# Optimization experiments

Measured on AMD Instinct MI355X. Metric: run time of the kernel, lower is better.

The kernel has to match this reference:

```python
import jax, jax.numpy as jnp
import numpy as np

B, C, H, W = 2, 1024, 64, 64
R, E, HE, T, K = 16, 4, 512, 3, 2


def setup_inputs() -> dict:
    key = jax.random.key(0)
    ks = jax.random.split(key, 12)
    s = 0.02
    return {
        "x": jax.random.normal(ks[0], (B, C, H, W), jnp.float32),
        "t": jax.random.normal(ks[1], (B, C, H, W), jnp.float32),
        "fc_w": jax.random.normal(ks[2], (C, 2 * C), jnp.float32) * s,
        "ln_g": jnp.ones((C,), jnp.float32),
        "ln_b": jnp.zeros((C,), jnp.float32),
        "f1_w1": jax.random.normal(ks[3], (C // R, C), jnp.float32) * s,
        "f1_b1": jnp.zeros((C // R,), jnp.float32),
        "f1_wa": jax.random.normal(ks[4], (C, C // R), jnp.float32) * s,
        "f1_ba": jnp.zeros((C,), jnp.float32),
        "f1_wb": jax.random.normal(ks[5], (C, C // R), jnp.float32) * s,
        "f1_bb": jnp.zeros((C,), jnp.float32),
        "w_gate": jax.random.normal(ks[6], (T, C, E), jnp.float32) * s,
        "e_w1": jax.random.normal(ks[7], (E, C, HE), jnp.float32) * s,
        "e_b1": jnp.zeros((E, HE), jnp.float32),
        "e_w2": jax.random.normal(ks[8], (E, HE, C), jnp.float32) * s,
        "e_b2": jnp.zeros((E, C), jnp.float32),
        "task_index": 1,
    }


def _cv_squared(v):
    eps = 1e-10
    return jnp.var(v, ddof=1) / (jnp.mean(v) ** 2 + eps)


def reference(x, t, fc_w, ln_g, ln_b, f1_w1, f1_b1, f1_wa, f1_ba, f1_wb, f1_bb,
              w_gate, e_w1, e_b1, e_w2, e_b2, task_index):
    b, c, h, w = x.shape
    n = h * w
    # MultiTaskGeneralFusion: SE-style dual-branch channel gating
    s = jnp.mean(x + t, axis=(2, 3))                        # [B, C]
    hid = jax.nn.relu(s @ f1_w1.T + f1_b1)                  # [B, C/r]
    a = hid @ f1_wa.T + f1_ba                               # [B, C]
    bb = hid @ f1_wb.T + f1_bb                              # [B, C]
    wts = jax.nn.softmax(jnp.stack([a, bb], axis=0), axis=0)  # [2, B, C]
    z = wts[0][:, :, None, None] * x + wts[1][:, :, None, None] * t
    # fused linear -> ReLU -> LayerNorm on concatenated tokens
    x3 = x.reshape(b, c, n).transpose(0, 2, 1)              # [B, N, C]
    t3 = t.reshape(b, c, n).transpose(0, 2, 1)
    y = jnp.concatenate([x3, t3], axis=-1)                  # [B, N, 2C]
    y = jax.nn.relu(jnp.einsum('bnd,cd->bnc', y, fc_w))     # [B, N, C]
    mu = jnp.mean(y, axis=-1, keepdims=True)
    var = jnp.mean((y - mu) ** 2, axis=-1, keepdims=True)
    y = (y - mu) * jax.lax.rsqrt(var + 1e-5) * ln_g + ln_b
    yf = y.reshape(b * n, c)                                # [BN, C]
    # MMoE top-k gating (eval mode: no gating noise)
    logits = yf @ w_gate[task_index]                        # [BN, E]
    top_logits, top_idx = jax.lax.top_k(logits, K)          # [BN, K]
    top_gates = jax.nn.softmax(top_logits, axis=-1)
    gates = jnp.zeros_like(logits).at[jnp.arange(b * n)[:, None], top_idx].set(top_gates)
    # dense expert compute, gated combine
    eh = jax.nn.relu(jnp.einsum('nc,ech->neh', yf, e_w1) + e_b1)   # [BN, E, HE]
    eo = jnp.einsum('neh,eho->neo', eh, e_w2) + e_b2               # [BN, E, C]
    ym = jnp.einsum('ne,neo->no', gates, eo)                        # [BN, C]
    importance = gates.sum(axis=0)
    load = (gates > 0).sum(axis=0).astype(jnp.float32)
    aux_loss = _cv_squared(importance) + _cv_squared(load)
    y4 = ym.reshape(b, n, c).transpose(0, 2, 1).reshape(b, c, h, w) + z
    return (y4, aux_loss)
```

## Files before the change

kernel.cpp:

```cpp
#include <hip/hip_runtime.h>
#include <cstddef>
#include <cstdint>

#define B_   2
#define C_   1024
#define N_   4096
#define M_   8192
#define K2_  2048
#define E_   4
#define HE_  512

typedef float f32x4 __attribute__((ext_vector_type(4)));
typedef short bf16x8 __attribute__((ext_vector_type(8)));
typedef _Float16 f16x8 __attribute__((ext_vector_type(8)));
typedef unsigned short u16x8 __attribute__((ext_vector_type(8)));

#define WAITV(N) asm volatile("s_waitcnt vmcnt(" #N ")" ::: "memory")
#define SBAR     __builtin_amdgcn_sched_barrier(0)

static __device__ __forceinline__ unsigned short f2bf(float f) {
  unsigned int u = __float_as_uint(f);
  u = u + 0x7fffu + ((u >> 16) & 1u);
  return (unsigned short)(u >> 16);
}

static __device__ __forceinline__ void gl_lds16(const void* g, void* l) {
  __builtin_amdgcn_global_load_lds(
      (const __attribute__((address_space(1))) void*)(uintptr_t)g,
      (__attribute__((address_space(3))) void*)(unsigned)(uintptr_t)l,
      16, 0, 0);
}

__global__ __launch_bounds__(256) void k_se_gate(const float* __restrict__ s,
                                                 const float* __restrict__ w1, const float* __restrict__ b1,
                                                 const float* __restrict__ wa, const float* __restrict__ ba,
                                                 const float* __restrict__ wb, const float* __restrict__ bbv,
                                                 float* __restrict__ wts0) {
  __shared__ float hid[2][64];
  const int t = threadIdx.x;
  if (t < 128) {
    const int b = t >> 6, r = t & 63;
    float acc = b1[r];
    const float* sp = s + b * C_;
    const float* wp = w1 + r * C_;
    for (int c = 0; c < C_; ++c) acc = fmaf(sp[c], wp[c], acc);
    hid[b][r] = fmaxf(acc, 0.f);
  }
  __syncthreads();
  for (int o = t; o < B_ * C_; o += 256) {
    const int b = o >> 10, c = o & 1023;
    float a = ba[c], bb = bbv[c];
    #pragma unroll 8
    for (int r = 0; r < 64; ++r) {
      const float h = hid[b][r];
      a  = fmaf(h, wa[c * 64 + r], a);
      bb = fmaf(h, wb[c * 64 + r], bb);
    }
    wts0[o] = 1.f / (1.f + expf(bb - a));
  }
}

__global__ __launch_bounds__(256) void k_prep_act(const float* __restrict__ x,
                                                  const float* __restrict__ t,
                                                  _Float16* __restrict__ ah,
                                                  _Float16* __restrict__ am,
                                                  float* __restrict__ spart) {
  __shared__ float tile[64][65];
  const int c0 = blockIdx.x * 64, n0 = blockIdx.y * 64, b = blockIdx.z;
  const float* xb = x + (size_t)b * (C_ * N_);
  const float* tb = t + (size_t)b * (C_ * N_);
  _Float16* ahb = ah + (size_t)b * (N_ * (size_t)K2_);
  _Float16* amb = am + (size_t)b * (N_ * (size_t)K2_);
  const int tid = threadIdx.x;
  const int prow = tid >> 2, pseg = tid & 3;
  float psum = 0.f;
  #pragma unroll
  for (int srcsel = 0; srcsel < 2; ++srcsel) {
    const float* src = srcsel ? tb : xb;
    const int koff = srcsel ? C_ : 0;
    if (srcsel) __syncthreads();
    #pragma unroll
    for (int p = 0; p < 4; ++p) {
      const int f = tid + p * 256;
      const int cr = f >> 4, nq = f & 15;
      const float4 v = *(const float4*)(src + (size_t)(c0 + cr) * N_ + n0 + nq * 4);
      tile[cr][nq * 4 + 0] = v.x; tile[cr][nq * 4 + 1] = v.y;
      tile[cr][nq * 4 + 2] = v.z; tile[cr][nq * 4 + 3] = v.w;
    }
    __syncthreads();
    {
      float a = 0.f;
      #pragma unroll
      for (int u = 0; u < 16; ++u) a += tile[prow][pseg * 16 + u];
      psum += a;
    }
    #pragma unroll
    for (int p = 0; p < 2; ++p) {
      const int f = tid + p * 256;
      const int mr = f >> 3, kq = f & 7;
      f16x8 hv, mv;
      #pragma unroll
      for (int u = 0; u < 8; ++u) {
        const float v = tile[kq * 8 + u][mr] * 64.f;
        const _Float16 h = (_Float16)v;
        hv[u] = h;
        mv[u] = (_Float16)(v - (float)h);
      }
      const size_t off = (size_t)(n0 + mr) * K2_ + koff + c0 + kq * 8;
      *(f16x8*)(ahb + off) = hv;
      *(f16x8*)(amb + off) = mv;
    }
  }
  psum += __shfl_xor(psum, 1);
  psum += __shfl_xor(psum, 2);
  if (pseg == 0)
    spart[((size_t)(b * C_ + c0 + prow)) * 64 + blockIdx.y] = psum;
}

__global__ __launch_bounds__(256) void k_reduce2(const float* __restrict__ spart,
                                                 float* __restrict__ s) {
  const int idx = blockIdx.x * 256 + threadIdx.x;
  const float* p = spart + (size_t)idx * 64;
  float acc = 0.f;
  #pragma unroll
  for (int j = 0; j < 64; ++j) acc += p[j];
  s[idx] = acc * (1.f / (float)N_);
}

__global__ __launch_bounds__(256) void k_prep_fcw(const float* __restrict__ w,
                                                  _Float16* __restrict__ wh,
                                                  _Float16* __restrict__ wm) {
  const size_t i = ((size_t)blockIdx.x * 256 + threadIdx.x) * 8;
  const float4 v0 = *(const float4*)(w + i);
  const float4 v1 = *(const float4*)(w + i + 4);
  const float vv[8] = {v0.x, v0.y, v0.z, v0.w, v1.x, v1.y, v1.z, v1.w};
  f16x8 hv, mv;
  #pragma unroll
  for (int u = 0; u < 8; ++u) {
    const float sv = vv[u] * 4096.f;
    const _Float16 h = (_Float16)sv;
    hv[u] = h;
    mv[u] = (_Float16)(sv - (float)h);
  }
  *(f16x8*)(wh + i) = hv;
  *(f16x8*)(wm + i) = mv;
}

__global__ __launch_bounds__(256) void k_prep_tr(const float* __restrict__ src, long long zs, int srs,
                                                 unsigned short* __restrict__ dst, long long zo, int drs) {
  __shared__ float tile[64][65];
  const int c0 = blockIdx.x * 64, r0 = blockIdx.y * 64, z = blockIdx.z;
  const float* s = src + (size_t)z * zs;
  unsigned short* d = dst + (size_t)z * zo;
  const int tid = threadIdx.x;
  #pragma unroll
  for (int p = 0; p < 4; ++p) {
    const int f = tid + p * 256;
    const int rr = f >> 4, cq = f & 15;
    const float4 v = *(const float4*)(s + (size_t)(r0 + rr) * srs + c0 + cq * 4);
    tile[rr][cq * 4 + 0] = v.x; tile[rr][cq * 4 + 1] = v.y;
    tile[rr][cq * 4 + 2] = v.z; tile[rr][cq * 4 + 3] = v.w;
  }
  __syncthreads();
  #pragma unroll
  for (int p = 0; p < 2; ++p) {
    const int f = tid + p * 256;
    const int cr = f >> 3, rq = f & 7;
    u16x8 o;
    #pragma unroll
    for (int u = 0; u < 8; ++u) o[u] = f2bf(tile[rq * 8 + u][cr]);
    *(u16x8*)(d + (size_t)(c0 + cr) * drs + r0 + rq * 8) = o;
  }
}

__global__ __launch_bounds__(512, 2) void k_fc_mfma(const _Float16* __restrict__ Ah,
                                                    const _Float16* __restrict__ Am,
                                                    const _Float16* __restrict__ Bh,
                                                    const _Float16* __restrict__ Bm,
                                                    float* __restrict__ y) {
  __shared__ __align__(16) char lds[2][49152];
  const int tid = threadIdx.x, w = tid >> 6, l = tid & 63;
  const int flat = blockIdx.x + blockIdx.y * 8;
  const int swz = (flat & 7) * 32 + (flat >> 3);
  const int n0 = (swz & 7) * 128, m0 = (swz >> 3) * 256;
  const int wr = w >> 1, wc = w & 1, lg = l >> 4, lr = l & 15;
  f32x4 acc[4][4] = {};

  auto LDA = [&](char* bufb, const _Float16* src, int roff, int k0, int q) {
    const int chunk = q * 512 + tid;
    const int kg = chunk >> 8, row = chunk & 255;
    gl_lds16(src + (size_t)(m0 + row) * K2_ + k0 + kg * 8,
             bufb + roff + (q * 512 + w * 64) * 16);
  };
  auto LDB = [&](char* bufb, const _Float16* src, int roff, int k0) {
    const int kg = tid >> 7, row = tid & 127;
    gl_lds16(src + (size_t)(n0 + row) * K2_ + k0 + kg * 8,
             bufb + roff + (w * 64) * 16);
  };

  LDA(&lds[0][0], Ah, 0, 0, 0);
  LDA(&lds[0][0], Ah, 0, 0, 1);
  LDB(&lds[0][0], Bh, 32768, 0);
  LDB(&lds[0][0], Bm, 40960, 0);
  LDA(&lds[0][0], Am, 16384, 0, 0);
  LDA(&lds[0][0], Am, 16384, 0, 1);

  f16x8 a_h[4], b_h[4], b_m[4], a_m[4];
  for (int t = 0; t < 63; ++t) {
    const int cur = t & 1;
    const char* bb = &lds[cur][0];
    char* nb = &lds[cur ^ 1][0];
    const int nk = (t + 1) * 32;
    WAITV(3); SBAR;
    __builtin_amdgcn_s_barrier();
    LDA(nb, Ah, 0, nk, 0);
    LDA(nb, Ah, 0, nk, 1);
    #pragma unroll
    for (int i = 0; i < 4; ++i)
      a_h[i] = *(const f16x8*)(bb + (lg * 256 + wr * 64 + i * 16 + lr) * 16);
    #pragma unroll
    for (int j = 0; j < 4; ++j)
      b_h[j] = *(const f16x8*)(bb + 32768 + (lg * 128 + wc * 64 + j * 16 + lr) * 16);
    __builtin_amdgcn_s_setprio(1);
    #pragma unroll
    for (int i = 0; i < 4; ++i)
      #pragma unroll
      for (int j = 0; j < 4; ++j)
        acc[i][j] = __builtin_amdgcn_mfma_f32_16x16x32_f16(a_h[i], b_h[j], acc[i][j], 0, 0, 0);
    __builtin_amdgcn_s_setprio(0);
    WAITV(4); SBAR;
    __builtin_amdgcn_s_barrier();
    LDB(nb, Bh, 32768, nk);
    LDB(nb, Bm, 40960, nk);
    #pragma unroll
    for (int j = 0; j < 4; ++j)
      b_m[j] = *(const f16x8*)(bb + 40960 + (lg * 128 + wc * 64 + j * 16 + lr) * 16);
    __builtin_amdgcn_s_setprio(1);
    #pragma unroll
    for (int i = 0; i < 4; ++i)
      #pragma unroll
      for (int j = 0; j < 4; ++j)
        acc[i][j] = __builtin_amdgcn_mfma_f32_16x16x32_f16(a_h[i], b_m[j], acc[i][j], 0, 0, 0);
    __builtin_amdgcn_s_setprio(0);
    WAITV(4); SBAR;
    __builtin_amdgcn_s_barrier();
    LDA(nb, Am, 16384, nk, 0);
    LDA(nb, Am, 16384, nk, 1);
    #pragma unroll
    for (int i = 0; i < 4; ++i)
      a_m[i] = *(const f16x8*)(bb + 16384 + (lg * 256 + wr * 64 + i * 16 + lr) * 16);
    __builtin_amdgcn_s_setprio(1);
    #pragma unroll
    for (int i = 0; i < 4; ++i)
      #pragma unroll
      for (int j = 0; j < 4; ++j)
        acc[i][j] = __builtin_amdgcn_mfma_f32_16x16x32_f16(a_m[i], b_h[j], acc[i][j], 0, 0, 0);
    __builtin_amdgcn_s_setprio(0);
  }
  {
    const char* bb = &lds[1][0];
    WAITV(3); SBAR;
    __builtin_amdgcn_s_barrier();
    #pragma unroll
    for (int i = 0; i < 4; ++i)
      a_h[i] = *(const f16x8*)(bb + (lg * 256 + wr * 64 + i * 16 + lr) * 16);
    #pragma unroll
    for (int j = 0; j < 4; ++j)
      b_h[j] = *(const f16x8*)(bb + 32768 + (lg * 128 + wc * 64 + j * 16 + lr) * 16);
    #pragma unroll
    for (int i = 0; i < 4; ++i)
      #pragma unroll
      for (int j = 0; j < 4; ++j)
        acc[i][j] = __builtin_amdgcn_mfma_f32_16x16x32_f16(a_h[i], b_h[j], acc[i][j], 0, 0, 0);
    WAITV(2); SBAR;
    __builtin_amdgcn_s_barrier();
    #pragma unroll
    for (int j = 0; j < 4; ++j)
      b_m[j] = *(const f16x8*)(bb + 40960 + (lg * 128 + wc * 64 + j * 16 + lr) * 16);
    #pragma unroll
    for (int i = 0; i < 4; ++i)
      #pragma unroll
      for (int j = 0; j < 4; ++j)
        acc[i][j] = __builtin_amdgcn_mfma_f32_16x16x32_f16(a_h[i], b_m[j], acc[i][j], 0, 0, 0);
    WAITV(0); SBAR;
    __builtin_amdgcn_s_barrier();
    #pragma unroll
    for (int i = 0; i < 4; ++i)
      a_m[i] = *(const f16x8*)(bb + 16384 + (lg * 256 + wr * 64 + i * 16 + lr) * 16);
    #pragma unroll
    for (int i = 0; i < 4; ++i)
      #pragma unroll
      for (int j = 0; j < 4; ++j)
        acc[i][j] = __builtin_amdgcn_mfma_f32_16x16x32_f16(a_m[i], b_h[j], acc[i][j], 0, 0, 0);
  }
  #pragma unroll
  for (int i = 0; i < 4; ++i) {
    const int mb = m0 + wr * 64 + i * 16 + lg * 4;
    #pragma unroll
    for (int j = 0; j < 4; ++j) {
      const int n = n0 + wc * 64 + j * 16 + lr;
      #pragma unroll
      for (int r = 0; r < 4; ++r)
        y[(size_t)(mb + r) * C_ + n] = fmaxf(acc[i][j][r] * (1.f / 262144.f), 0.f);
    }
  }
}

__global__ __launch_bounds__(256) void k_ln_topk(const float* __restrict__ y,
                                                 const float* __restrict__ lng, const float* __restrict__ lnb,
                                                 const float* __restrict__ wg, const int* __restrict__ taskp,
                                                 unsigned short* __restrict__ yf, float* __restrict__ gates) {
  const int wv = threadIdx.x >> 6, ln = threadIdx.x & 63;
  const int m = blockIdx.x * 4 + wv;
  const float* yr = y + (size_t)m * C_;
  float4 v[4];
  #pragma unroll
  for (int ch = 0; ch < 4; ++ch) v[ch] = *(const float4*)(yr + ch * 256 + ln * 4);
  float sum = 0.f;
  #pragma unroll
  for (int ch = 0; ch < 4; ++ch) sum += (v[ch].x + v[ch].y) + (v[ch].z + v[ch].w);
  #pragma unroll
  for (int o = 32; o; o >>= 1) sum += __shfl_down(sum, o);
  sum = __shfl(sum, 0);
  const float mu = sum * (1.f / 1024.f);
  float q = 0.f;
  #pragma unroll
  for (int ch = 0; ch < 4; ++ch) {
    const float dx = v[ch].x - mu, dy = v[ch].y - mu, dz = v[ch].z - mu, dw = v[ch].w - mu;
    q += (dx * dx + dy * dy) + (dz * dz + dw * dw);
  }
  #pragma unroll
  for (int o = 32; o; o >>= 1) q += __shfl_down(q, o);
  q = __shfl(q, 0);
  const float rstd = rsqrtf(q * (1.f / 1024.f) + 1e-5f);
  const float* wrow = wg + (size_t)(*taskp) * (C_ * E_);
  float l0 = 0.f, l1 = 0.f, l2 = 0.f, l3 = 0.f;
  #pragma unroll
  for (int ch = 0; ch < 4; ++ch) {
    const int c = ch * 256 + ln * 4;
    const float4 gg = *(const float4*)(lng + c);
    const float4 bv = *(const float4*)(lnb + c);
    float f[4];
    f[0] = (v[ch].x - mu) * rstd * gg.x + bv.x;
    f[1] = (v[ch].y - mu) * rstd * gg.y + bv.y;
    f[2] = (v[ch].z - mu) * rstd * gg.z + bv.z;
    f[3] = (v[ch].w - mu) * rstd * gg.w + bv.w;
    uint2 pk;
    pk.x = (unsigned)f2bf(f[0]) | ((unsigned)f2bf(f[1]) << 16);
    pk.y = (unsigned)f2bf(f[2]) | ((unsigned)f2bf(f[3]) << 16);
    *(uint2*)(yf + (size_t)m * C_ + c) = pk;
    #pragma unroll
    for (int i = 0; i < 4; ++i) {
      const float4 we = *(const float4*)(wrow + (size_t)(c + i) * 4);
      l0 = fmaf(f[i], we.x, l0); l1 = fmaf(f[i], we.y, l1);
      l2 = fmaf(f[i], we.z, l2); l3 = fmaf(f[i], we.w, l3);
    }
  }
  #pragma unroll
  for (int o = 32; o; o >>= 1) {
    l0 += __shfl_down(l0, o); l1 += __shfl_down(l1, o);
    l2 += __shfl_down(l2, o); l3 += __shfl_down(l3, o);
  }
  if (ln == 0) {
    const float L[4] = {l0, l1, l2, l3};
    int i1 = 0; float best = L[0];
    #pragma unroll
    for (int e = 1; e < 4; ++e) if (L[e] > best) { best = L[e]; i1 = e; }
    int i2 = -1; float s2 = 0.f;
    #pragma unroll
    for (int e = 0; e < 4; ++e) if (e != i1 && (i2 < 0 || L[e] > s2)) { s2 = L[e]; i2 = e; }
    const float g1 = 1.f / (1.f + expf(s2 - best));
    const float g2 = 1.f - g1;
    float4 gv;
    gv.x = (i1 == 0) ? g1 : ((i2 == 0) ? g2 : 0.f);
    gv.y = (i1 == 1) ? g1 : ((i2 == 1) ? g2 : 0.f);
    gv.z = (i1 == 2) ? g1 : ((i2 == 2) ? g2 : 0.f);
    gv.w = (i1 == 3) ? g1 : ((i2 == 3) ? g2 : 0.f);
    *(float4*)(gates + (size_t)m * 4) = gv;
  }
}

__global__ __launch_bounds__(256) void k_moe1_mfma(const unsigned short* __restrict__ yf,
                                                   const short* __restrict__ Bw,
                                                   const float* __restrict__ b1,
                                                   const float* __restrict__ gates,
                                                   unsigned short* __restrict__ ehg) {
  __shared__ __align__(16) char lds[3][16384];
  const int tid = threadIdx.x, w = tid >> 6, l = tid & 63;
  const int flat = blockIdx.x + blockIdx.y * 16;
  const int swz = (flat & 7) * 128 + (flat >> 3);
  const int n0 = (swz & 15) * 128, m0 = (swz >> 4) * 128;
  const int wr = w >> 1, wc = w & 1, lg = l >> 4, lr = l & 15;
  f32x4 acc[4][4] = {};
  const int sg = tid >> 7, sr = tid & 127;
  const size_t ga0 = (size_t)(m0 + sr) * C_ + sg * 8;
  const size_t gb0 = (size_t)(n0 + sr) * C_ + sg * 8;

  auto STAGE = [&](int buf, int k0) {
    char* b = &lds[buf][0] + w * 1024;
    gl_lds16(yf + ga0 + k0, b);
    gl_lds16(yf + ga0 + 16 + k0, b + 4096);
    gl_lds16(Bw + gb0 + k0, b + 8192);
    gl_lds16(Bw + gb0 + 16 + k0, b + 12288);
  };

  STAGE(0, 0);
  STAGE(1, 32);
  for (int it = 0; it < 32; ++it) {
    const int cur = it % 3;
    if (it < 31) { WAITV(4); } else { WAITV(0); }
    SBAR;
    __builtin_amdgcn_s_barrier();
    if (it < 30) STAGE((it + 2) % 3, (it + 2) * 32);
    const char* bb = &lds[cur][0];
    bf16x8 af[4], bfr[4];
    #pragma unroll
    for (int i = 0; i < 4; ++i)
      af[i] = *(const bf16x8*)(bb + lg * 2048 + (wr * 64 + i * 16 + lr) * 16);
    #pragma unroll
    for (int j = 0; j < 4; ++j)
      bfr[j] = *(const bf16x8*)(bb + 8192 + lg * 2048 + (wc * 64 + j * 16 + lr) * 16);
    __builtin_amdgcn_s_setprio(1);
    #pragma unroll
    for (int i = 0; i < 4; ++i)
      #pragma unroll
      for (int j = 0; j < 4; ++j)
        acc[i][j] = __builtin_amdgcn_mfma_f32_16x16x32_bf16(af[i], bfr[j], acc[i][j], 0, 0, 0);
    __builtin_amdgcn_s_setprio(0);
  }
  const int e0 = n0 >> 9;
  #pragma unroll
  for (int j = 0; j < 4; ++j) {
    const int n = n0 + wc * 64 + j * 16 + lr;
    const float bias = b1[e0 * HE_ + (n & 511)];
    #pragma unroll
    for (int i = 0; i < 4; ++i) {
      const int mb = m0 + wr * 64 + i * 16 + lg * 4;
      #pragma unroll
      for (int r = 0; r < 4; ++r) {
        const float g = gates[(size_t)(mb + r) * 4 + e0];
        const float v = fmaxf(acc[i][j][r] + bias, 0.f) * g;
        ehg[(size_t)(mb + r) * K2_ + n] = f2bf(v);
      }
    }
  }
}

__global__ __launch_bounds__(256) void k_moe2_mfma(const short* __restrict__ Aeh,
                                                   const short* __restrict__ Bw,
                                                   const float* __restrict__ b2,
                                                   const float* __restrict__ gates,
                                                   float* __restrict__ ym) {
  __shared__ __align__(16) char lds[3][16384];
  const int tid = threadIdx.x, w = tid >> 6, l = tid & 63;
  const int flat = blockIdx.x + blockIdx.y * 8;
  const int swz = (flat & 7) * 64 + (flat >> 3);
  const int n0 = (swz & 7) * 128, m0 = (swz >> 3) * 128;
  const int wr = w >> 1, wc = w & 1, lg = l >> 4, lr = l & 15;
  f32x4 acc[4][4] = {};
  const int sg = tid >> 7, sr = tid & 127;
  const size_t ga0 = (size_t)(m0 + sr) * K2_ + sg * 8;
  const size_t gb0 = (size_t)(n0 + sr) * K2_ + sg * 8;

  auto STAGE = [&](int buf, int k0) {
    char* b = &lds[buf][0] + w * 1024;
    gl_lds16(Aeh + ga0 + k0, b);
    gl_lds16(Aeh + ga0 + 16 + k0, b + 4096);
    gl_lds16(Bw + gb0 + k0, b + 8192);
    gl_lds16(Bw + gb0 + 16 + k0, b + 12288);
  };

  STAGE(0, 0);
  STAGE(1, 32);
  for (int it = 0; it < 64; ++it) {
    const int cur = it % 3;
    if (it < 63) { WAITV(4); } else { WAITV(0); }
    SBAR;
    __builtin_amdgcn_s_barrier();
    if (it < 62) STAGE((it + 2) % 3, (it + 2) * 32);
    const char* bb = &lds[cur][0];
    bf16x8 af[4], bfr[4];
    #pragma unroll
    for (int i = 0; i < 4; ++i)
      af[i] = *(const bf16x8*)(bb + lg * 2048 + (wr * 64 + i * 16 + lr) * 16);
    #pragma unroll
    for (int j = 0; j < 4; ++j)
      bfr[j] = *(const bf16x8*)(bb + 8192 + lg * 2048 + (wc * 64 + j * 16 + lr) * 16);
    __builtin_amdgcn_s_setprio(1);
    #pragma unroll
    for (int i = 0; i < 4; ++i)
      #pragma unroll
      for (int j = 0; j < 4; ++j)
        acc[i][j] = __builtin_amdgcn_mfma_f32_16x16x32_bf16(af[i], bfr[j], acc[i][j], 0, 0, 0);
    __builtin_amdgcn_s_setprio(0);
  }
  float bb2[4][4];
  #pragma unroll
  for (int j = 0; j < 4; ++j) {
    const int n = n0 + wc * 64 + j * 16 + lr;
    #pragma unroll
    for (int e = 0; e < 4; ++e) bb2[j][e] = b2[e * C_ + n];
  }
  #pragma unroll
  for (int i = 0; i < 4; ++i) {
    const int mb = m0 + wr * 64 + i * 16 + lg * 4;
    #pragma unroll
    for (int r = 0; r < 4; ++r) {
      const float4 g = *(const float4*)(gates + (size_t)(mb + r) * 4);
      #pragma unroll
      for (int j = 0; j < 4; ++j) {
        const int n = n0 + wc * 64 + j * 16 + lr;
        ym[(size_t)(mb + r) * C_ + n] =
            acc[i][j][r] + g.x * bb2[j][0] + g.y * bb2[j][1] + g.z * bb2[j][2] + g.w * bb2[j][3];
      }
    }
  }
}

__global__ __launch_bounds__(256) void k_aux(const float* __restrict__ gates, float* __restrict__ outp) {
  const int t = threadIdx.x;
  float imp[4] = {0, 0, 0, 0}, ld[4] = {0, 0, 0, 0};
  for (int m = t; m < M_; m += 256) {
    const float4 g = *(const float4*)(gates + (size_t)m * 4);
    imp[0] += g.x; imp[1] += g.y; imp[2] += g.z; imp[3] += g.w;
    ld[0] += (g.x > 0.f) ? 1.f : 0.f; ld[1] += (g.y > 0.f) ? 1.f : 0.f;
    ld[2] += (g.z > 0.f) ? 1.f : 0.f; ld[3] += (g.w > 0.f) ? 1.f : 0.f;
  }
  __shared__ float red[8][4];
  const int wv = t >> 6, ln = t & 63;
  #pragma unroll
  for (int e = 0; e < 4; ++e) {
    float a = imp[e], b = ld[e];
    #pragma unroll
    for (int o = 32; o; o >>= 1) { a += __shfl_down(a, o); b += __shfl_down(b, o); }
    if (ln == 0) { red[e][wv] = a; red[4 + e][wv] = b; }
  }
  __syncthreads();
  if (t == 0) {
    float I[4], L[4];
    #pragma unroll
    for (int e = 0; e < 4; ++e) {
      I[e] = red[e][0] + red[e][1] + red[e][2] + red[e][3];
      L[e] = red[4 + e][0] + red[4 + e][1] + red[4 + e][2] + red[4 + e][3];
    }
    const float mi = (I[0] + I[1] + I[2] + I[3]) * 0.25f;
    const float vi = ((I[0] - mi) * (I[0] - mi) + (I[1] - mi) * (I[1] - mi) +
                      (I[2] - mi) * (I[2] - mi) + (I[3] - mi) * (I[3] - mi)) / 3.f;
    const float ml = (L[0] + L[1] + L[2] + L[3]) * 0.25f;
    const float vl = ((L[0] - ml) * (L[0] - ml) + (L[1] - ml) * (L[1] - ml) +
                      (L[2] - ml) * (L[2] - ml) + (L[3] - ml) * (L[3] - ml)) / 3.f;
    *outp = vi / (mi * mi + 1e-10f) + vl / (ml * ml + 1e-10f);
  }
}

__global__ __launch_bounds__(256) void k_final(const float* __restrict__ ym,
                                               const float* __restrict__ x, const float* __restrict__ t,
                                               const float* __restrict__ wts0, float* __restrict__ out) {
  __shared__ float tile[64][65];
  const int c0 = blockIdx.x * 64, n0 = blockIdx.y * 64, b = blockIdx.z;
  const int tid = threadIdx.x;
  #pragma unroll
  for (int p = 0; p < 4; ++p) {
    const int f = tid + p * 256;
    const int row = f >> 4, cq = f & 15;
    const float4 v = *(const float4*)(ym + (size_t)(b * N_ + n0 + row) * C_ + c0 + cq * 4);
    tile[row][cq * 4 + 0] = v.x; tile[row][cq * 4 + 1] = v.y;
    tile[row][cq * 4 + 2] = v.z; tile[row][cq * 4 + 3] = v.w;
  }
  __syncthreads();
  #pragma unroll
  for (int p = 0; p < 4; ++p) {
    const int f = tid + p * 256;
    const int cr = f >> 4, nq = f & 15;
    const int c = c0 + cr;
    const float w0 = wts0[b * C_ + c];
    const float w1 = 1.f - w0;
    const size_t idx = (size_t)(b * C_ + c) * N_ + n0 + nq * 4;
    const float4 xv = *(const float4*)(x + idx);
    const float4 tv = *(const float4*)(t + idx);
    float4 o;
    o.x = tile[nq * 4 + 0][cr] + w0 * xv.x + w1 * tv.x;
    o.y = tile[nq * 4 + 1][cr] + w0 * xv.y + w1 * tv.y;
    o.z = tile[nq * 4 + 2][cr] + w0 * xv.z + w1 * tv.z;
    o.w = tile[nq * 4 + 3][cr] + w0 * xv.w + w1 * tv.w;
    *(float4*)(out + idx) = o;
  }
}

extern "C" void kernel_launch(void* const* d_in, const int* in_sizes, int n_in,
                              void* d_out, int out_size, void* d_ws, size_t ws_size,
                              hipStream_t stream) {
  const float* x     = (const float*)d_in[0];
  const float* t     = (const float*)d_in[1];
  const float* fc_w  = (const float*)d_in[2];
  const float* ln_g  = (const float*)d_in[3];
  const float* ln_b  = (const float*)d_in[4];
  const float* f1_w1 = (const float*)d_in[5];
  const float* f1_b1 = (const float*)d_in[6];
  const float* f1_wa = (const float*)d_in[7];
  const float* f1_ba = (const float*)d_in[8];
  const float* f1_wb = (const float*)d_in[9];
  const float* f1_bb = (const float*)d_in[10];
  const float* w_gate = (const float*)d_in[11];
  const float* e_w1  = (const float*)d_in[12];
  const float* e_b1  = (const float*)d_in[13];
  const float* e_w2  = (const float*)d_in[14];
  const float* e_b2  = (const float*)d_in[15];
  const int*   task  = (const int*)d_in[16];
  float* out = (float*)d_out;

  char* ws = (char*)d_ws;
  float*          y     = (float*)ws;
  float*          spart = (float*)ws;
  _Float16*       ah    = (_Float16*)(ws + 33554432);
  _Float16*       am    = (_Float16*)(ws + 67108864);
  unsigned short* yf    = (unsigned short*)(ws + 33554432);
  unsigned short* ehg   = (unsigned short*)(ws + 50331648);
  _Float16* wh  = (_Float16*)(ws + 100663296);
  _Float16* wm  = (_Float16*)(ws + 104857600);
  short*    w1t = (short*)(ws + 109051904);
  short*    w2t = (short*)(ws + 113246208);
  float* sbuf  = (float*)(ws + 117440512);
  float* wts0  = (float*)(ws + 117448704);
  float* gates = (float*)(ws + 117456896);

  k_prep_fcw<<<1024, 256, 0, stream>>>(fc_w, wh, wm);
  k_prep_tr<<<dim3(8, 16, 4), 256, 0, stream>>>(e_w1, 524288LL, 512, (unsigned short*)w1t, 524288LL, 1024);
  k_prep_tr<<<dim3(16, 8, 4), 256, 0, stream>>>(e_w2, 524288LL, 1024, (unsigned short*)w2t, 512LL, 2048);
  k_prep_act<<<dim3(16, 64, 2), 256, 0, stream>>>(x, t, ah, am, spart);
  k_reduce2<<<8, 256, 0, stream>>>(spart, sbuf);
  k_se_gate<<<1, 256, 0, stream>>>(sbuf, f1_w1, f1_b1, f1_wa, f1_ba, f1_wb, f1_bb, wts0);
  k_fc_mfma<<<dim3(8, 32), 512, 0, stream>>>(ah, am, wh, wm, y);
  k_ln_topk<<<M_ / 4, 256, 0, stream>>>(y, ln_g, ln_b, w_gate, task, yf, gates);
  k_moe1_mfma<<<dim3(16, 64), 256, 0, stream>>>(yf, w1t, e_b1, gates, ehg);
  k_moe2_mfma<<<dim3(8, 64), 256, 0, stream>>>((const short*)ehg, w2t, e_b2, gates, y);
  k_aux<<<1, 256, 0, stream>>>(gates, out + (size_t)B_ * C_ * N_);
  k_final<<<dim3(C_ / 64, N_ / 64, B_), 256, 0, stream>>>(y, x, t, wts0, out);
}
```

Before: 407.6 us.

## Route tokens sparsely to top-2 experts instead of dense expert compute

Adds a scheduling kernel that compacts, per expert, the list of tokens with nonzero gate and builds a tile work list. The two expert GEMMs now run only over the routed tokens of each expert (about half of the dense work with top-2 of 4), writing gated bf16 expert outputs per routed slot. The final kernel gathers and sums up to two expert rows per token via a position map. The cost is a single-block scheduling kernel, indirect row gathers in the first GEMM, and bf16 rounding of the expert outputs before combining.

```diff
diff --git a/kernel.cpp b/kernel.cpp
--- a/kernel.cpp
+++ b/kernel.cpp
@@ -22,6 +22,9 @@
   unsigned int u = __float_as_uint(f);
   u = u + 0x7fffu + ((u >> 16) & 1u);
   return (unsigned short)(u >> 16);
+}
+static __device__ __forceinline__ float bf2f(unsigned short h) {
+  return __uint_as_float(((unsigned int)h) << 16);
 }
 
 static __device__ __forceinline__ void gl_lds16(const void* g, void* l) {
@@ -380,21 +383,75 @@
   }
 }
 
+__global__ __launch_bounds__(256) void k_sched(const float* __restrict__ gates,
+                                               int* __restrict__ idx,
+                                               int* __restrict__ pos4,
+                                               int* __restrict__ meta) {
+  __shared__ unsigned long long smask[4][128];
+  __shared__ int scnt[4], sbase[4];
+  const int w = threadIdx.x >> 6, lane = threadIdx.x & 63;
+  {
+    const int e = w;
+    int cnt = 0;
+    for (int it0 = 0; it0 < 128; it0 += 8) {
+      float gv[8];
+      #pragma unroll
+      for (int u = 0; u < 8; ++u)
+        gv[u] = gates[(size_t)((it0 + u) * 64 + lane) * 4 + e];
+      #pragma unroll
+      for (int u = 0; u < 8; ++u) {
+        const unsigned long long mask = __ballot(gv[u] > 0.f);
+        if (lane == 0) smask[e][it0 + u] = mask;
+        cnt += (int)__popcll(mask);
+      }
+    }
+    if (lane == 0) scnt[e] = cnt;
+  }
+  __syncthreads();
+  if (threadIdx.x == 0) {
+    int b = 0;
+    for (int e = 0; e < 4; ++e) { sbase[e] = b; meta[e] = scnt[e]; meta[4 + e] = b; b += scnt[e]; }
+    int nt = 0;
+    for (int e = 0; e < 4; ++e)
+      for (int k = 0; k < scnt[e]; k += 128) { meta[16 + 2 * nt] = e; meta[17 + 2 * nt] = k; ++nt; }
+    meta[8] = nt;
+  }
+  __syncthreads();
+  {
+    const int e = w;
+    int cnt = 0;
+    const int b = sbase[e];
+    for (int it = 0; it < 128; ++it) {
+      const unsigned long long mask = smask[e][it];
+      const int tok = it * 64 + lane;
+      const bool act = (mask >> lane) & 1ull;
+      const int pos = cnt + (int)__popcll(mask & ((1ull << lane) - 1ull));
+      if (act) { idx[b + pos] = tok; pos4[(size_t)tok * 4 + e] = b + pos; }
+      else pos4[(size_t)tok * 4 + e] = -1;
+      cnt += (int)__popcll(mask);
+    }
+  }
+}
+
 __global__ __launch_bounds__(256) void k_moe1_mfma(const unsigned short* __restrict__ yf,
                                                    const short* __restrict__ Bw,
                                                    const float* __restrict__ b1,
-                                                   const float* __restrict__ gates,
-                                                   unsigned short* __restrict__ ehg) {
+                                                   const int* __restrict__ idx,
+                                                   const int* __restrict__ meta,
+                                                   unsigned short* __restrict__ eh) {
   __shared__ __align__(16) char lds[3][16384];
   const int tid = threadIdx.x, w = tid >> 6, l = tid & 63;
-  const int flat = blockIdx.x + blockIdx.y * 16;
-  const int swz = (flat & 7) * 128 + (flat >> 3);
-  const int n0 = (swz & 15) * 128, m0 = (swz >> 4) * 128;
+  if ((int)blockIdx.y >= meta[8]) return;
+  const int e = meta[16 + 2 * blockIdx.y], rstart = meta[17 + 2 * blockIdx.y];
+  const int cntE = meta[e], baseE = meta[4 + e];
+  const int n0 = blockIdx.x * 128;
   const int wr = w >> 1, wc = w & 1, lg = l >> 4, lr = l & 15;
   f32x4 acc[4][4] = {};
   const int sg = tid >> 7, sr = tid & 127;
-  const size_t ga0 = (size_t)(m0 + sr) * C_ + sg * 8;
-  const size_t gb0 = (size_t)(n0 + sr) * C_ + sg * 8;
+  const int rl = rstart + sr;
+  const int tokA = idx[baseE + (rl < cntE ? rl : cntE - 1)];
+  const size_t ga0 = (size_t)tokA * C_ + sg * 8;
+  const size_t gb0 = (size_t)(e * HE_ + n0 + sr) * C_ + sg * 8;
 
   auto STAGE = [&](int buf, int k0) {
     char* b = &lds[buf][0] + w * 1024;
@@ -428,56 +485,60 @@
         acc[i][j] = __builtin_amdgcn_mfma_f32_16x16x32_bf16(af[i], bfr[j], acc[i][j], 0, 0, 0);
     __builtin_amdgcn_s_setprio(0);
   }
-  const int e0 = n0 >> 9;
   #pragma unroll
   for (int j = 0; j < 4; ++j) {
-    const int n = n0 + wc * 64 + j * 16 + lr;
-    const float bias = b1[e0 * HE_ + (n & 511)];
+    const int col = n0 + wc * 64 + j * 16 + lr;
+    const float bias = b1[e * HE_ + col];
     #pragma unroll
     for (int i = 0; i < 4; ++i) {
-      const int mb = m0 + wr * 64 + i * 16 + lg * 4;
+      const int mb = wr * 64 + i * 16 + lg * 4;
       #pragma unroll
       for (int r = 0; r < 4; ++r) {
-        const float g = gates[(size_t)(mb + r) * 4 + e0];
-        const float v = fmaxf(acc[i][j][r] + bias, 0.f) * g;
-        ehg[(size_t)(mb + r) * K2_ + n] = f2bf(v);
+        const int rr = rstart + mb + r;
+        if (rr < cntE) {
+          const float v = fmaxf(acc[i][j][r] + bias, 0.f);
+          eh[(size_t)(baseE + rr) * HE_ + col] = f2bf(v);
+        }
       }
     }
   }
 }
 
-__global__ __launch_bounds__(256) void k_moe2_mfma(const short* __restrict__ Aeh,
+__global__ __launch_bounds__(256) void k_moe2_mfma(const unsigned short* __restrict__ eh,
                                                    const short* __restrict__ Bw,
                                                    const float* __restrict__ b2,
                                                    const float* __restrict__ gates,
-                                                   float* __restrict__ ym) {
+                                                   const int* __restrict__ idx,
+                                                   const int* __restrict__ meta,
+                                                   unsigned short* __restrict__ eo) {
   __shared__ __align__(16) char lds[3][16384];
   const int tid = threadIdx.x, w = tid >> 6, l = tid & 63;
-  const int flat = blockIdx.x + blockIdx.y * 8;
-  const int swz = (flat & 7) * 64 + (flat >> 3);
-  const int n0 = (swz & 7) * 128, m0 = (swz >> 3) * 128;
+  if ((int)blockIdx.y >= meta[8]) return;
+  const int e = meta[16 + 2 * blockIdx.y], rstart = meta[17 + 2 * blockIdx.y];
+  const int cntE = meta[e], baseE = meta[4 + e];
+  const int n0 = blockIdx.x * 128;
   const int wr = w >> 1, wc = w & 1, lg = l >> 4, lr = l & 15;
   f32x4 acc[4][4] = {};
   const int sg = tid >> 7, sr = tid & 127;
-  const size_t ga0 = (size_t)(m0 + sr) * K2_ + sg * 8;
-  const size_t gb0 = (size_t)(n0 + sr) * K2_ + sg * 8;
+  const size_t ga0 = (size_t)(baseE + rstart + sr) * HE_ + sg * 8;
+  const size_t gb0 = (size_t)(n0 + sr) * K2_ + e * HE_ + sg * 8;
 
   auto STAGE = [&](int buf, int k0) {
     char* b = &lds[buf][0] + w * 1024;
-    gl_lds16(Aeh + ga0 + k0, b);
-    gl_lds16(Aeh + ga0 + 16 + k0, b + 4096);
+    gl_lds16(eh + ga0 + k0, b);
+    gl_lds16(eh + ga0 + 16 + k0, b + 4096);
     gl_lds16(Bw + gb0 + k0, b + 8192);
     gl_lds16(Bw + gb0 + 16 + k0, b + 12288);
   };
 
   STAGE(0, 0);
   STAGE(1, 32);
-  for (int it = 0; it < 64; ++it) {
+  for (int it = 0; it < 16; ++it) {
     const int cur = it % 3;
-    if (it < 63) { WAITV(4); } else { WAITV(0); }
+    if (it < 15) { WAITV(4); } else { WAITV(0); }
     SBAR;
     __builtin_amdgcn_s_barrier();
-    if (it < 62) STAGE((it + 2) % 3, (it + 2) * 32);
+    if (it < 14) STAGE((it + 2) % 3, (it + 2) * 32);
     const char* bb = &lds[cur][0];
     bf16x8 af[4], bfr[4];
     #pragma unroll
@@ -494,24 +555,21 @@
         acc[i][j] = __builtin_amdgcn_mfma_f32_16x16x32_bf16(af[i], bfr[j], acc[i][j], 0, 0, 0);
     __builtin_amdgcn_s_setprio(0);
   }
-  float bb2[4][4];
-  #pragma unroll
-  for (int j = 0; j < 4; ++j) {
-    const int n = n0 + wc * 64 + j * 16 + lr;
-    #pragma unroll
-    for (int e = 0; e < 4; ++e) bb2[j][e] = b2[e * C_ + n];
-  }
   #pragma unroll
   for (int i = 0; i < 4; ++i) {
-    const int mb = m0 + wr * 64 + i * 16 + lg * 4;
+    const int mb = wr * 64 + i * 16 + lg * 4;
     #pragma unroll
     for (int r = 0; r < 4; ++r) {
-      const float4 g = *(const float4*)(gates + (size_t)(mb + r) * 4);
-      #pragma unroll
-      for (int j = 0; j < 4; ++j) {
-        const int n = n0 + wc * 64 + j * 16 + lr;
-        ym[(size_t)(mb + r) * C_ + n] =
-            acc[i][j][r] + g.x * bb2[j][0] + g.y * bb2[j][1] + g.z * bb2[j][2] + g.w * bb2[j][3];
+      const int rr = rstart + mb + r;
+      if (rr < cntE) {
+        const int tok = idx[baseE + rr];
+        const float g = gates[(size_t)tok * 4 + e];
+        #pragma unroll
+        for (int j = 0; j < 4; ++j) {
+          const int n = n0 + wc * 64 + j * 16 + lr;
+          const float val = (acc[i][j][r] + b2[e * C_ + n]) * g;
+          eo[(size_t)(baseE + rr) * C_ + n] = f2bf(val);
+        }
       }
     }
   }
@@ -553,7 +611,8 @@
   }
 }
 
-__global__ __launch_bounds__(256) void k_final(const float* __restrict__ ym,
+__global__ __launch_bounds__(256) void k_final(const unsigned short* __restrict__ eo,
+                                               const int* __restrict__ pos4,
                                                const float* __restrict__ x, const float* __restrict__ t,
                                                const float* __restrict__ wts0, float* __restrict__ out) {
   __shared__ float tile[64][65];
@@ -563,9 +622,19 @@
   for (int p = 0; p < 4; ++p) {
     const int f = tid + p * 256;
     const int row = f >> 4, cq = f & 15;
-    const float4 v = *(const float4*)(ym + (size_t)(b * N_ + n0 + row) * C_ + c0 + cq * 4);
-    tile[row][cq * 4 + 0] = v.x; tile[row][cq * 4 + 1] = v.y;
-    tile[row][cq * 4 + 2] = v.z; tile[row][cq * 4 + 3] = v.w;
+    const int m = b * N_ + n0 + row;
+    const int4 pp = *(const int4*)(pos4 + (size_t)m * 4);
+    float v0 = 0.f, v1 = 0.f, v2 = 0.f, v3 = 0.f;
+    const int pa[4] = {pp.x, pp.y, pp.z, pp.w};
+    #pragma unroll
+    for (int e = 0; e < 4; ++e) {
+      if (pa[e] >= 0) {
+        const ushort4 u = *(const ushort4*)(eo + (size_t)pa[e] * C_ + c0 + cq * 4);
+        v0 += bf2f(u.x); v1 += bf2f(u.y); v2 += bf2f(u.z); v3 += bf2f(u.w);
+      }
+    }
+    tile[row][cq * 4 + 0] = v0; tile[row][cq * 4 + 1] = v1;
+    tile[row][cq * 4 + 2] = v2; tile[row][cq * 4 + 3] = v3;
   }
   __syncthreads();
   #pragma unroll
@@ -575,15 +644,15 @@
     const int c = c0 + cr;
     const float w0 = wts0[b * C_ + c];
     const float w1 = 1.f - w0;
-    const size_t idx = (size_t)(b * C_ + c) * N_ + n0 + nq * 4;
-    const float4 xv = *(const float4*)(x + idx);
-    const float4 tv = *(const float4*)(t + idx);
+    const size_t idx2 = (size_t)(b * C_ + c) * N_ + n0 + nq * 4;
+    const float4 xv = *(const float4*)(x + idx2);
+    const float4 tv = *(const float4*)(t + idx2);
     float4 o;
     o.x = tile[nq * 4 + 0][cr] + w0 * xv.x + w1 * tv.x;
     o.y = tile[nq * 4 + 1][cr] + w0 * xv.y + w1 * tv.y;
     o.z = tile[nq * 4 + 2][cr] + w0 * xv.z + w1 * tv.z;
     o.w = tile[nq * 4 + 3][cr] + w0 * xv.w + w1 * tv.w;
-    *(float4*)(out + idx) = o;
+    *(float4*)(out + idx2) = o;
   }
 }
 
@@ -612,10 +681,14 @@
   char* ws = (char*)d_ws;
   float*          y     = (float*)ws;
   float*          spart = (float*)ws;
+  unsigned short* eo    = (unsigned short*)ws;
   _Float16*       ah    = (_Float16*)(ws + 33554432);
   _Float16*       am    = (_Float16*)(ws + 67108864);
   unsigned short* yf    = (unsigned short*)(ws + 33554432);
-  unsigned short* ehg   = (unsigned short*)(ws + 50331648);
+  unsigned short* eh    = (unsigned short*)(ws + 50331648);
+  int*            idx   = (int*)(ws + 67108864);
+  int*            pos4  = (int*)(ws + 67174400);
+  int*            meta  = (int*)(ws + 67305472);
   _Float16* wh  = (_Float16*)(ws + 100663296);
   _Float16* wm  = (_Float16*)(ws + 104857600);
   short*    w1t = (short*)(ws + 109051904);
@@ -632,8 +705,9 @@
   k_se_gate<<<1, 256, 0, stream>>>(sbuf, f1_w1, f1_b1, f1_wa, f1_ba, f1_wb, f1_bb, wts0);
   k_fc_mfma<<<dim3(8, 32), 512, 0, stream>>>(ah, am, wh, wm, y);
   k_ln_topk<<<M_ / 4, 256, 0, stream>>>(y, ln_g, ln_b, w_gate, task, yf, gates);
-  k_moe1_mfma<<<dim3(16, 64), 256, 0, stream>>>(yf, w1t, e_b1, gates, ehg);
-  k_moe2_mfma<<<dim3(8, 64), 256, 0, stream>>>((const short*)ehg, w2t, e_b2, gates, y);
+  k_sched<<<1, 256, 0, stream>>>(gates, idx, pos4, meta);
+  k_moe1_mfma<<<dim3(4, 132), 256, 0, stream>>>(yf, w1t, e_b1, idx, meta, eh);
+  k_moe2_mfma<<<dim3(8, 132), 256, 0, stream>>>(eh, w2t, e_b2, gates, idx, meta, eo);
   k_aux<<<1, 256, 0, stream>>>(gates, out + (size_t)B_ * C_ * N_);
-  k_final<<<dim3(C_ / 64, N_ / 64, B_), 256, 0, stream>>>(y, x, t, wts0, out);
-}
+  k_final<<<dim3(C_ / 64, N_ / 64, B_), 256, 0, stream>>>(eo, pos4, x, t, wts0, out);
+}
```

Result: no change. 413.5 us (+1.4%).
